# Kernel optimization log

Measured on AMD Instinct MI355X. Metric: run time of the kernel, lower is better.

The kernel has to match this reference:

```python
import jax, jax.numpy as jnp
import numpy as np

MASK_VALUE = -1e6  # torch code uses -1000000.0, not -inf


def setup_inputs() -> dict:
    key = jax.random.key(0)
    k1, k2, k3, k4 = jax.random.split(key, 4)
    B, Nq, Nk, d = 32, 2048, 2048, 128
    return {
        "querys": jax.random.normal(k1, (B, Nq, d), dtype=jnp.float32),
        "keys": jax.random.normal(k2, (B, Nk, d), dtype=jnp.float32),
        "values": jax.random.normal(k3, (B, Nk, d), dtype=jnp.float32),
        "valid_seq_len": jax.random.randint(k4, (B,), 1, Nk + 1, dtype=jnp.int32),
    }


def reference(querys, keys, values, valid_seq_len):
    # querys: [B, Nq, d], keys/values: [B, Nk, d], valid_seq_len: [B]
    d = querys.shape[-1]
    scale = 1.0 / jnp.sqrt(jnp.asarray(d, dtype=querys.dtype))
    # scores: [B, Nq, Nk]
    scores = jnp.einsum("bqd,bkd->bqk", querys, keys) * scale
    Nk = keys.shape[1]
    # mask key positions >= valid length (per batch, broadcast over queries)
    mask = jnp.arange(Nk, dtype=jnp.int32)[None, None, :] < valid_seq_len[:, None, None]
    scores = jnp.where(mask, scores, jnp.asarray(MASK_VALUE, dtype=scores.dtype))
    attn = jax.nn.softmax(scores, axis=-1)
    # dropout prob = 0.0 -> identity
    out = jnp.einsum("bqk,bkd->bqd", attn, values)
    return out
```

## Files before the change

kernel.cpp:

```cpp
#include <hip/hip_runtime.h>
#include <cstdint>
#include <math.h>

typedef unsigned short ushort_t;
typedef unsigned int uint_t;
typedef __bf16 v8bf __attribute__((ext_vector_type(8)));
typedef float v16f __attribute__((ext_vector_type(16)));

constexpr int B_SZ = 32, NQ = 2048, NK = 2048, DH = 128;
constexpr int BK = 64;
constexpr int TILE_E = 8192;
constexpr float QSCALE = 0.12751880226116815f;
constexpr float M2 = 17.312340490667561f;

__device__ __forceinline__ float4 ld4f(const float* p) {
  return *reinterpret_cast<const float4*>(p);
}
__device__ __forceinline__ uint4 ld4u(const ushort_t* p) {
  return *reinterpret_cast<const uint4*>(p);
}

__device__ inline v8bf cvt8(const float* __restrict__ p) {
  float4 f0 = ld4f(p);
  float4 f1 = ld4f(p + 4);
  v8bf r;
  r[0] = (__bf16)f0.x; r[1] = (__bf16)f0.y; r[2] = (__bf16)f0.z; r[3] = (__bf16)f0.w;
  r[4] = (__bf16)f1.x; r[5] = (__bf16)f1.y; r[6] = (__bf16)f1.z; r[7] = (__bf16)f1.w;
  return r;
}

__device__ inline v8bf cvt8s(const float* __restrict__ p, float s) {
  float4 f0 = ld4f(p);
  float4 f1 = ld4f(p + 4);
  v8bf r;
  r[0] = (__bf16)(f0.x * s); r[1] = (__bf16)(f0.y * s);
  r[2] = (__bf16)(f0.z * s); r[3] = (__bf16)(f0.w * s);
  r[4] = (__bf16)(f1.x * s); r[5] = (__bf16)(f1.y * s);
  r[6] = (__bf16)(f1.z * s); r[7] = (__bf16)(f1.w * s);
  return r;
}

__device__ __forceinline__ uint_t pk2(float a, float b) {
  const ushort_t ua = __builtin_bit_cast(ushort_t, (__bf16)a);
  const ushort_t ub = __builtin_bit_cast(ushort_t, (__bf16)b);
  return (uint_t)ua | ((uint_t)ub << 16);
}

__global__ __launch_bounds__(256) void prep_kv(const float* __restrict__ K,
                                               const float* __restrict__ V,
                                               ushort_t* __restrict__ Kf,
                                               ushort_t* __restrict__ Vf) {
  __shared__ __align__(16) ushort_t st[64 * 128];
  const int b = blockIdx.y, tq = blockIdx.x, k0 = tq * 64, t = threadIdx.x;
  const int l32 = t & 31, g = t >> 5;
  {
    const float* Kb = K + ((size_t)(b * NK + k0)) * DH;
    ushort_t* out = Kf + ((size_t)(b * 32 + tq)) * TILE_E;
    for (int c = 0; c < 4; ++c) {
      const int id = g * 4 + c;
      const int kb = id >> 4, ks = (id >> 1) & 7, hi = id & 1;
      v8bf v = cvt8(Kb + (size_t)(kb * 32 + l32) * DH + (2 * ks + hi) * 8);
      *reinterpret_cast<v8bf*>(out + (size_t)id * 256 + l32 * 8) = v;
    }
  }
  for (int c = 0; c < 4; ++c) {
    const int row = (t >> 4) + 16 * c;
    const int col = (t & 15) * 8;
    v8bf v = cvt8(V + ((size_t)(b * NK + k0 + row)) * DH + col);
    const int chunk = (col >> 3) ^ ((row >> 3) & 7);
    *reinterpret_cast<v8bf*>(&st[row * 128 + chunk * 8]) = v;
  }
  __syncthreads();
  {
    ushort_t* out = Vf + ((size_t)(b * 32 + tq)) * TILE_E;
    for (int c = 0; c < 4; ++c) {
      const int f = g + 8 * c;
      const int nb = f & 3, hi = (f >> 2) & 1, ksg = f >> 3;
      const int d = nb * 32 + l32;
      alignas(16) ushort_t tmp[8];
      for (int j = 0; j < 8; ++j) {
        const int row = ksg * 16 + hi * 8 + j;
        const int elem = (d & 7) | (((d >> 3) ^ ((row >> 3) & 7)) << 3);
        tmp[j] = st[row * 128 + elem];
      }
      *reinterpret_cast<uint4*>(out + ((ksg * 2 + hi) * 4 + nb) * 256 + l32 * 8) =
          *reinterpret_cast<const uint4*>(tmp);
    }
  }
}

__device__ __forceinline__ void qk_sm(const ushort_t* kt, int l32, int hi, int k0n,
                                      int valid, const v8bf* qf, float& ls0,
                                      float& ls1, uint4& pa0, uint4& pa1,
                                      uint4& pa2, uint4& pa3) {
  const bool part = (k0n + BK > valid);
#pragma unroll
  for (int kb = 0; kb < 2; ++kb) {
    const ushort_t* base = kt + kb * 4096 + hi * 256 + l32 * 8;
    const uint4 kf0 = ld4u(base + 0 * 512);
    const uint4 kf1 = ld4u(base + 1 * 512);
    const uint4 kf2 = ld4u(base + 2 * 512);
    const uint4 kf3 = ld4u(base + 3 * 512);
    const uint4 kf4 = ld4u(base + 4 * 512);
    const uint4 kf5 = ld4u(base + 5 * 512);
    const uint4 kf6 = ld4u(base + 6 * 512);
    const uint4 kf7 = ld4u(base + 7 * 512);
    v16f sa;
#pragma unroll
    for (int r = 0; r < 16; ++r) sa[r] = 0.f;
    __builtin_amdgcn_s_setprio(1);
    sa = __builtin_amdgcn_mfma_f32_32x32x16_bf16(__builtin_bit_cast(v8bf, kf0), qf[0], sa, 0, 0, 0);
    sa = __builtin_amdgcn_mfma_f32_32x32x16_bf16(__builtin_bit_cast(v8bf, kf1), qf[1], sa, 0, 0, 0);
    sa = __builtin_amdgcn_mfma_f32_32x32x16_bf16(__builtin_bit_cast(v8bf, kf2), qf[2], sa, 0, 0, 0);
    sa = __builtin_amdgcn_mfma_f32_32x32x16_bf16(__builtin_bit_cast(v8bf, kf3), qf[3], sa, 0, 0, 0);
    sa = __builtin_amdgcn_mfma_f32_32x32x16_bf16(__builtin_bit_cast(v8bf, kf4), qf[4], sa, 0, 0, 0);
    sa = __builtin_amdgcn_mfma_f32_32x32x16_bf16(__builtin_bit_cast(v8bf, kf5), qf[5], sa, 0, 0, 0);
    sa = __builtin_amdgcn_mfma_f32_32x32x16_bf16(__builtin_bit_cast(v8bf, kf6), qf[6], sa, 0, 0, 0);
    sa = __builtin_amdgcn_mfma_f32_32x32x16_bf16(__builtin_bit_cast(v8bf, kf7), qf[7], sa, 0, 0, 0);
    __builtin_amdgcn_s_setprio(0);
    float p[16];
#pragma unroll
    for (int r = 0; r < 16; ++r) {
      const int crow = (r & 3) + 8 * (r >> 2) + 4 * hi;
      float x = sa[r];
      if (part) x = (k0n + kb * 32 + crow < valid) ? x : -1e30f;
      float e;
      asm("v_exp_f32 %0, %1" : "=v"(e) : "v"(x - M2));
      p[r] = e;
      if (r < 8) ls0 += e; else ls1 += e;
    }
#pragma unroll
    for (int q2 = 0; q2 < 2; ++q2) {
      uint_t A0 = pk2(p[8 * q2 + 0], p[8 * q2 + 1]);
      uint_t A1 = pk2(p[8 * q2 + 2], p[8 * q2 + 3]);
      uint_t B0 = pk2(p[8 * q2 + 4], p[8 * q2 + 5]);
      uint_t B1 = pk2(p[8 * q2 + 6], p[8 * q2 + 7]);
      asm("v_permlane32_swap_b32 %0, %1" : "+v"(A0), "+v"(B0));
      asm("v_permlane32_swap_b32 %0, %1" : "+v"(A1), "+v"(B1));
      uint4 fw;
      fw.x = A0; fw.y = A1; fw.z = B0; fw.w = B1;
      if (kb == 0) { if (q2 == 0) pa0 = fw; else pa1 = fw; }
      else         { if (q2 == 0) pa2 = fw; else pa3 = fw; }
    }
  }
}

__device__ __forceinline__ void pv4(const ushort_t* vt, int l32, int hi,
                                    const uint4 paf, int ksg, v16f* o) {
  const ushort_t* vb = vt + ksg * 2048 + hi * 1024 + l32 * 8;
  const uint4 vf0 = ld4u(vb + 0 * 256);
  const uint4 vf1 = ld4u(vb + 1 * 256);
  const uint4 vf2 = ld4u(vb + 2 * 256);
  const uint4 vf3 = ld4u(vb + 3 * 256);
  const v8bf pa = __builtin_bit_cast(v8bf, paf);
  __builtin_amdgcn_s_setprio(1);
  o[0] = __builtin_amdgcn_mfma_f32_32x32x16_bf16(pa, __builtin_bit_cast(v8bf, vf0), o[0], 0, 0, 0);
  o[1] = __builtin_amdgcn_mfma_f32_32x32x16_bf16(pa, __builtin_bit_cast(v8bf, vf1), o[1], 0, 0, 0);
  o[2] = __builtin_amdgcn_mfma_f32_32x32x16_bf16(pa, __builtin_bit_cast(v8bf, vf2), o[2], 0, 0, 0);
  o[3] = __builtin_amdgcn_mfma_f32_32x32x16_bf16(pa, __builtin_bit_cast(v8bf, vf3), o[3], 0, 0, 0);
  __builtin_amdgcn_s_setprio(0);
}

__global__ __launch_bounds__(256, 2) void attn(const float* __restrict__ Q,
                                               const ushort_t* __restrict__ Kf,
                                               const ushort_t* __restrict__ Vf,
                                               const int* __restrict__ vsl,
                                               float* __restrict__ Out) {
  __shared__ int s_ord[32];
  __shared__ float mO[2][4096];
  __shared__ float sRS[2][32];

  const int t = threadIdx.x;
  const int lane = t & 63, w = t >> 6;
  const int wq = w & 1, pr = w >> 1;
  const int hi = lane >> 5, l32 = lane & 31;

  if (t < 32) {
    const int cx = (vsl[t] + 63) >> 6;
    int rank = 0;
    for (int y = 0; y < 32; ++y) {
      const int cy = (vsl[y] + 63) >> 6;
      rank += (cy > cx) || (cy == cx && y < t);
    }
    s_ord[rank] = t;
  }
  __syncthreads();
  const int n = (int)blockIdx.x;
  const int ci = n & 255, cj = n >> 8;
  const int rk = (cj == 0) ? ci : (cj == 1) ? 511 - ci : (cj == 2) ? 512 + ci : 1023 - ci;
  const int b = s_ord[rk >> 5];
  const int qt = rk & 31;

  const int q0 = qt * 64;
  const int valid = vsl[b];
  const int nt = (valid + BK - 1) / BK;
  const int myNt = (nt + 1 - pr) >> 1;

  v8bf qf[8];
  {
    const float* qp = Q + ((size_t)(b * NQ + q0 + wq * 32 + l32)) * DH + hi * 8;
#pragma unroll
    for (int ks = 0; ks < 8; ++ks) qf[ks] = cvt8s(qp + ks * 16, QSCALE);
  }

  v16f o[4];
#pragma unroll
  for (int nb = 0; nb < 4; ++nb)
#pragma unroll
    for (int r = 0; r < 16; ++r) o[nb][r] = 0.f;
  float ls0 = 0.f, ls1 = 0.f;

  const ushort_t* Kb = Kf + (size_t)b * 32 * TILE_E;
  const ushort_t* Vb = Vf + (size_t)b * 32 * TILE_E;

  for (int i = 0; i < myNt; ++i) {
    const int tile = 2 * i + pr;
    const ushort_t* kt = Kb + (size_t)tile * TILE_E;
    const ushort_t* vt = Vb + (size_t)tile * TILE_E;
    uint4 pa0, pa1, pa2, pa3;
    qk_sm(kt, l32, hi, tile * BK, valid, qf, ls0, ls1, pa0, pa1, pa2, pa3);
    pv4(vt, l32, hi, pa0, 0, o);
    pv4(vt, l32, hi, pa1, 1, o);
    pv4(vt, l32, hi, pa2, 2, o);
    pv4(vt, l32, hi, pa3, 3, o);
  }

  const float lsw = ls0 + ls1;
  const float rsw = lsw + __shfl_xor(lsw, 32);
  if (pr == 1) {
#pragma unroll
    for (int nb = 0; nb < 4; ++nb)
#pragma unroll
      for (int r = 0; r < 16; ++r)
        mO[wq][(nb * 16 + r) * 64 + lane] = o[nb][r];
    if (hi == 0) sRS[wq][l32] = rsw;
  }
  __syncthreads();
  if (pr == 0) {
    const float rs = rsw + sRS[wq][l32];
#pragma unroll
    for (int nb = 0; nb < 4; ++nb)
#pragma unroll
      for (int r = 0; r < 16; ++r) o[nb][r] += mO[wq][(nb * 16 + r) * 64 + lane];
    const float inv_own = 1.0f / rs;
#pragma unroll
    for (int r = 0; r < 16; ++r) {
      const int crow = (r & 3) + 8 * (r >> 2) + 4 * hi;
      const float inv = __shfl(inv_own, crow);
      float* op = Out + ((size_t)(b * NQ + q0 + wq * 32 + crow)) * DH + l32;
#pragma unroll
      for (int nb = 0; nb < 4; ++nb) op[nb * 32] = o[nb][r] * inv;
    }
  }
}

extern "C" void kernel_launch(void* const* d_in, const int* in_sizes, int n_in,
                              void* d_out, int out_size, void* d_ws, size_t ws_size,
                              hipStream_t stream) {
  const float* Q = (const float*)d_in[0];
  const float* K = (const float*)d_in[1];
  const float* V = (const float*)d_in[2];
  const int* vsl = (const int*)d_in[3];
  float* Out = (float*)d_out;

  ushort_t* Kf = (ushort_t*)d_ws;
  ushort_t* Vf = Kf + (size_t)B_SZ * 32 * TILE_E;

  prep_kv<<<dim3(NK / 64, B_SZ), dim3(256), 0, stream>>>(K, V, Kf, Vf);
  attn<<<dim3(1024), dim3(256), 0, stream>>>(Q, Kf, Vf, vsl, Out);
}
```

Baseline: 196.1 us.

## Software-pipeline K fragment loads across tiles with double-buffered registers

Restructures the main loop so the K fragments for the next tile and for the second half of the current tile are loaded from global memory before the current softmax/pack and MFMA work, using two register sets that alternate through a manually unrolled loop. The aim is to hide global load latency behind compute instead of stalling at the start of each tile. The cost is 64 more VGPRs of live fragment data per lane, which risks spills or lower occupancy under the 2-blocks-per-CU launch bound. The prefetch index is clamped to the last tile, so the final iteration issues a redundant load.

```diff
diff --git a/kernel.cpp b/kernel.cpp
--- a/kernel.cpp
+++ b/kernel.cpp
@@ -89,60 +89,49 @@
   }
 }
 
-__device__ __forceinline__ void qk_sm(const ushort_t* kt, int l32, int hi, int k0n,
-                                      int valid, const v8bf* qf, float& ls0,
-                                      float& ls1, uint4& pa0, uint4& pa1,
-                                      uint4& pa2, uint4& pa3) {
-  const bool part = (k0n + BK > valid);
-#pragma unroll
-  for (int kb = 0; kb < 2; ++kb) {
-    const ushort_t* base = kt + kb * 4096 + hi * 256 + l32 * 8;
-    const uint4 kf0 = ld4u(base + 0 * 512);
-    const uint4 kf1 = ld4u(base + 1 * 512);
-    const uint4 kf2 = ld4u(base + 2 * 512);
-    const uint4 kf3 = ld4u(base + 3 * 512);
-    const uint4 kf4 = ld4u(base + 4 * 512);
-    const uint4 kf5 = ld4u(base + 5 * 512);
-    const uint4 kf6 = ld4u(base + 6 * 512);
-    const uint4 kf7 = ld4u(base + 7 * 512);
-    v16f sa;
-#pragma unroll
-    for (int r = 0; r < 16; ++r) sa[r] = 0.f;
-    __builtin_amdgcn_s_setprio(1);
-    sa = __builtin_amdgcn_mfma_f32_32x32x16_bf16(__builtin_bit_cast(v8bf, kf0), qf[0], sa, 0, 0, 0);
-    sa = __builtin_amdgcn_mfma_f32_32x32x16_bf16(__builtin_bit_cast(v8bf, kf1), qf[1], sa, 0, 0, 0);
-    sa = __builtin_amdgcn_mfma_f32_32x32x16_bf16(__builtin_bit_cast(v8bf, kf2), qf[2], sa, 0, 0, 0);
-    sa = __builtin_amdgcn_mfma_f32_32x32x16_bf16(__builtin_bit_cast(v8bf, kf3), qf[3], sa, 0, 0, 0);
-    sa = __builtin_amdgcn_mfma_f32_32x32x16_bf16(__builtin_bit_cast(v8bf, kf4), qf[4], sa, 0, 0, 0);
-    sa = __builtin_amdgcn_mfma_f32_32x32x16_bf16(__builtin_bit_cast(v8bf, kf5), qf[5], sa, 0, 0, 0);
-    sa = __builtin_amdgcn_mfma_f32_32x32x16_bf16(__builtin_bit_cast(v8bf, kf6), qf[6], sa, 0, 0, 0);
-    sa = __builtin_amdgcn_mfma_f32_32x32x16_bf16(__builtin_bit_cast(v8bf, kf7), qf[7], sa, 0, 0, 0);
-    __builtin_amdgcn_s_setprio(0);
-    float p[16];
-#pragma unroll
-    for (int r = 0; r < 16; ++r) {
-      const int crow = (r & 3) + 8 * (r >> 2) + 4 * hi;
-      float x = sa[r];
-      if (part) x = (k0n + kb * 32 + crow < valid) ? x : -1e30f;
-      float e;
-      asm("v_exp_f32 %0, %1" : "=v"(e) : "v"(x - M2));
-      p[r] = e;
-      if (r < 8) ls0 += e; else ls1 += e;
-    }
-#pragma unroll
-    for (int q2 = 0; q2 < 2; ++q2) {
-      uint_t A0 = pk2(p[8 * q2 + 0], p[8 * q2 + 1]);
-      uint_t A1 = pk2(p[8 * q2 + 2], p[8 * q2 + 3]);
-      uint_t B0 = pk2(p[8 * q2 + 4], p[8 * q2 + 5]);
-      uint_t B1 = pk2(p[8 * q2 + 6], p[8 * q2 + 7]);
-      asm("v_permlane32_swap_b32 %0, %1" : "+v"(A0), "+v"(B0));
-      asm("v_permlane32_swap_b32 %0, %1" : "+v"(A1), "+v"(B1));
-      uint4 fw;
-      fw.x = A0; fw.y = A1; fw.z = B0; fw.w = B1;
-      if (kb == 0) { if (q2 == 0) pa0 = fw; else pa1 = fw; }
-      else         { if (q2 == 0) pa2 = fw; else pa3 = fw; }
-    }
-  }
+__device__ __forceinline__ v16f mfma8(uint4 f0, uint4 f1, uint4 f2, uint4 f3,
+                                      uint4 f4, uint4 f5, uint4 f6, uint4 f7,
+                                      const v8bf* qf) {
+  v16f sa;
+#pragma unroll
+  for (int r = 0; r < 16; ++r) sa[r] = 0.f;
+  __builtin_amdgcn_s_setprio(1);
+  sa = __builtin_amdgcn_mfma_f32_32x32x16_bf16(__builtin_bit_cast(v8bf, f0), qf[0], sa, 0, 0, 0);
+  sa = __builtin_amdgcn_mfma_f32_32x32x16_bf16(__builtin_bit_cast(v8bf, f1), qf[1], sa, 0, 0, 0);
+  sa = __builtin_amdgcn_mfma_f32_32x32x16_bf16(__builtin_bit_cast(v8bf, f2), qf[2], sa, 0, 0, 0);
+  sa = __builtin_amdgcn_mfma_f32_32x32x16_bf16(__builtin_bit_cast(v8bf, f3), qf[3], sa, 0, 0, 0);
+  sa = __builtin_amdgcn_mfma_f32_32x32x16_bf16(__builtin_bit_cast(v8bf, f4), qf[4], sa, 0, 0, 0);
+  sa = __builtin_amdgcn_mfma_f32_32x32x16_bf16(__builtin_bit_cast(v8bf, f5), qf[5], sa, 0, 0, 0);
+  sa = __builtin_amdgcn_mfma_f32_32x32x16_bf16(__builtin_bit_cast(v8bf, f6), qf[6], sa, 0, 0, 0);
+  sa = __builtin_amdgcn_mfma_f32_32x32x16_bf16(__builtin_bit_cast(v8bf, f7), qf[7], sa, 0, 0, 0);
+  __builtin_amdgcn_s_setprio(0);
+  return sa;
+}
+
+__device__ __forceinline__ void smpack(const v16f& sa, int kbase, int valid,
+                                       bool part, int hi, float& ls0, float& ls1,
+                                       uint4& paX, uint4& paY) {
+  float p[16];
+#pragma unroll
+  for (int r = 0; r < 16; ++r) {
+    const int crow = (r & 3) + 8 * (r >> 2) + 4 * hi;
+    float x = sa[r];
+    if (part) x = (kbase + crow < valid) ? x : -1e30f;
+    float e;
+    asm("v_exp_f32 %0, %1" : "=v"(e) : "v"(x - M2));
+    p[r] = e;
+    if (r < 8) ls0 += e; else ls1 += e;
+  }
+  uint_t A0 = pk2(p[0], p[1]), A1 = pk2(p[2], p[3]);
+  uint_t B0 = pk2(p[4], p[5]), B1 = pk2(p[6], p[7]);
+  asm("v_permlane32_swap_b32 %0, %1" : "+v"(A0), "+v"(B0));
+  asm("v_permlane32_swap_b32 %0, %1" : "+v"(A1), "+v"(B1));
+  paX.x = A0; paX.y = A1; paX.z = B0; paX.w = B1;
+  uint_t C0 = pk2(p[8], p[9]), C1 = pk2(p[10], p[11]);
+  uint_t D0 = pk2(p[12], p[13]), D1 = pk2(p[14], p[15]);
+  asm("v_permlane32_swap_b32 %0, %1" : "+v"(C0), "+v"(D0));
+  asm("v_permlane32_swap_b32 %0, %1" : "+v"(C1), "+v"(D1));
+  paY.x = C0; paY.y = C1; paY.z = D0; paY.w = D1;
 }
 
 __device__ __forceinline__ void pv4(const ushort_t* vt, int l32, int hi,
@@ -161,6 +150,46 @@
   __builtin_amdgcn_s_setprio(0);
 }
 
+#define LDK8(A0, A1, A2, A3, A4, A5, A6, A7, KT, KB)            \
+  do {                                                          \
+    const ushort_t* b_ = (KT) + (KB)*4096 + hi * 256 + l32 * 8; \
+    A0 = ld4u(b_ + 0 * 512);                                    \
+    A1 = ld4u(b_ + 1 * 512);                                    \
+    A2 = ld4u(b_ + 2 * 512);                                    \
+    A3 = ld4u(b_ + 3 * 512);                                    \
+    A4 = ld4u(b_ + 4 * 512);                                    \
+    A5 = ld4u(b_ + 5 * 512);                                    \
+    A6 = ld4u(b_ + 6 * 512);                                    \
+    A7 = ld4u(b_ + 7 * 512);                                    \
+  } while (0)
+
+#define TILE_BODY(U0, U1, U2, U3, U4, U5, U6, U7,                           \
+                  P0, P1, P2, P3, P4, P5, P6, P7, I)                        \
+  do {                                                                      \
+    const int tile_ = 2 * (I) + pr;                                         \
+    const ushort_t* kt_ = Kb + (size_t)tile_ * TILE_E;                      \
+    const ushort_t* vt_ = Vb + (size_t)tile_ * TILE_E;                      \
+    const int k0n_ = tile_ * BK;                                            \
+    const bool part_ = (k0n_ + BK > valid);                                 \
+    v16f sa0_ = mfma8(U0, U1, U2, U3, U4, U5, U6, U7, qf);                  \
+    uint4 t0_, t1_, t2_, t3_, t4_, t5_, t6_, t7_;                           \
+    LDK8(t0_, t1_, t2_, t3_, t4_, t5_, t6_, t7_, kt_, 1);                   \
+    uint4 pa0_, pa1_, pa2_, pa3_;                                           \
+    smpack(sa0_, k0n_, valid, part_, hi, ls0, ls1, pa0_, pa1_);             \
+    v16f sa1_ = mfma8(t0_, t1_, t2_, t3_, t4_, t5_, t6_, t7_, qf);          \
+    {                                                                       \
+      int nt_ = 2 * ((I) + 1) + pr;                                         \
+      nt_ = nt_ <= 31 ? nt_ : 31;        \
+      const ushort_t* nk_ = Kb + (size_t)nt_ * TILE_E;                      \
+      LDK8(P0, P1, P2, P3, P4, P5, P6, P7, nk_, 0);                         \
+    }                                                                       \
+    smpack(sa1_, k0n_ + 32, valid, part_, hi, ls0, ls1, pa2_, pa3_);        \
+    pv4(vt_, l32, hi, pa0_, 0, o);                                          \
+    pv4(vt_, l32, hi, pa1_, 1, o);                                          \
+    pv4(vt_, l32, hi, pa2_, 2, o);                                          \
+    pv4(vt_, l32, hi, pa3_, 3, o);                                          \
+  } while (0)
+
 __global__ __launch_bounds__(256, 2) void attn(const float* __restrict__ Q,
                                                const ushort_t* __restrict__ Kf,
                                                const ushort_t* __restrict__ Vf,
@@ -213,16 +242,19 @@
   const ushort_t* Kb = Kf + (size_t)b * 32 * TILE_E;
   const ushort_t* Vb = Vf + (size_t)b * 32 * TILE_E;
 
-  for (int i = 0; i < myNt; ++i) {
-    const int tile = 2 * i + pr;
-    const ushort_t* kt = Kb + (size_t)tile * TILE_E;
-    const ushort_t* vt = Vb + (size_t)tile * TILE_E;
-    uint4 pa0, pa1, pa2, pa3;
-    qk_sm(kt, l32, hi, tile * BK, valid, qf, ls0, ls1, pa0, pa1, pa2, pa3);
-    pv4(vt, l32, hi, pa0, 0, o);
-    pv4(vt, l32, hi, pa1, 1, o);
-    pv4(vt, l32, hi, pa2, 2, o);
-    pv4(vt, l32, hi, pa3, 3, o);
+  uint4 a0, a1, a2, a3, a4, a5, a6, a7;
+  uint4 b0, b1, b2, b3, b4, b5, b6, b7;
+  {
+    const ushort_t* kt0 = Kb + (size_t)pr * TILE_E;
+    LDK8(a0, a1, a2, a3, a4, a5, a6, a7, kt0, 0);
+  }
+  int i = 0;
+  while (i < myNt) {
+    TILE_BODY(a0, a1, a2, a3, a4, a5, a6, a7, b0, b1, b2, b3, b4, b5, b6, b7, i);
+    ++i;
+    if (i >= myNt) break;
+    TILE_BODY(b0, b1, b2, b3, b4, b5, b6, b7, a0, a1, a2, a3, a4, a5, a6, a7, i);
+    ++i;
   }
 
   const float lsw = ls0 + ls1;
```

Result: no change. 193.4 us (-1.4%).
